# Performance work log

Measured on AMD Instinct MI355X. Metric: run time of the kernel, lower is better.

Reference implementation:

```python
import jax, jax.numpy as jnp
import numpy as np

B, L, D, R = 8, 2048, 2048, 256
K = R if R % 2 == 1 else (R - 1 if R > 1 else 1)  # torch kernel-size rule -> 255


def setup_inputs() -> dict:
    key = jax.random.key(0)
    ks = jax.random.split(key, 6)
    x = jax.random.normal(ks[0], (B, L, D), dtype=jnp.float32)
    ln_gamma = jnp.ones((D,), jnp.float32)
    ln_beta = jnp.zeros((D,), jnp.float32)
    P_shared = jax.random.normal(ks[1], (D, R), jnp.float32) / np.float32(np.sqrt(D))
    dlt_T = jax.random.normal(ks[2], (R, R), jnp.float32) / np.float32(np.sqrt(R))
    phi_w = jax.random.normal(ks[3], (R,), jnp.float32)  # nn.Linear(1, r, bias=False) weight
    phi_bias = jnp.zeros((L, R), jnp.float32)            # created as zeros_like(phi_det)
    toep_params = jnp.ones((K,), jnp.float32) / np.float32(K)
    Wq = jax.random.normal(ks[4], (R, D), jnp.float32) / np.float32(np.sqrt(R))  # delta_Q: r->d
    bq = jnp.zeros((D,), jnp.float32)
    g_logit = jnp.array([-1.0, 0.0], jnp.float32)
    return {"x": x, "ln_gamma": ln_gamma, "ln_beta": ln_beta, "P_shared": P_shared,
            "dlt_T": dlt_T, "phi_w": phi_w, "phi_bias": phi_bias,
            "toep_params": toep_params, "Wq": Wq, "bq": bq, "g_logit": g_logit,
            "step": 5000}


def _layernorm(x, g, b, eps=1e-5):
    m = jnp.mean(x, -1, keepdims=True)
    v = jnp.mean((x - m) ** 2, -1, keepdims=True)
    return (x - m) * jax.lax.rsqrt(v + eps) * g + b


def _phi_det(Ll, Rr, dtype):
    # assumed phi_logic(t, L, r): DCT-II style deterministic phase table, shape (L, r)
    t = jnp.arange(Ll, dtype=dtype)[:, None]
    k = jnp.arange(Rr, dtype=dtype)[None, :]
    return jnp.cos(jnp.pi * (t + 0.5) * k / Ll)


def reference(x, ln_gamma, ln_beta, P_shared, dlt_T, phi_w, phi_bias,
              toep_params, Wq, bq, g_logit, step):
    Bb, Ll, Dd = x.shape
    Rr = P_shared.shape[1]
    x_norm = _layernorm(x, ln_gamma, ln_beta)
    phi_det = _phi_det(Ll, Rr, x.dtype)                      # (L, r)
    feat = jnp.mean(x_norm, -1, keepdims=True)               # (B, L, 1)
    phi_data = jnp.mean(feat * phi_w[None, None, :], axis=0)  # (L, r)
    det_scale = min(step / 2000.0, 1.0)                      # static Python scalar
    phi = det_scale * phi_det + phi_bias + phi_data          # (L, r)
    scale = jnp.sum(phi, axis=1) / jnp.float32(Rr)           # (L,)
    u = jnp.einsum('bld,dr->blr', x_norm, P_shared)          # SharedProj.forward_P
    z = jnp.einsum('blr,sr->bls', u, dlt_T)                  # DLT: fixed spectral transform
    # Toeplitz conv1d across spectral channels, padding 'same' (cross-correlation, as torch)
    zf = z.reshape(Bb * Ll, 1, Rr)
    mixed = jax.lax.conv_general_dilated(zf, toep_params[None, None, :], (1,), 'SAME',
                                         dimension_numbers=('NCH', 'OIH', 'NCH'))
    z_mixed = mixed.reshape(Bb, Ll, Rr)
    y = jnp.einsum('blr,rd->bld', z_mixed, Wq) + bq          # delta_Q
    g = jax.nn.sigmoid(g_logit)
    g = jnp.repeat(g, Dd // g.shape[0])                      # repeat_interleave to d_model
    # scale has L elements, broadcast over the FEATURE dim (L == d_model by construction)
    return g[None, None, :] * y * scale[None, None, :]
```

## Files before the change

kernel.cpp:

```cpp
#include <hip/hip_runtime.h>
#include <cstdint>
#include <math.h>

#define B_ 8
#define L_ 2048
#define D_ 2048
#define R_ 256

typedef __bf16 bf16x8 __attribute__((ext_vector_type(8)));
typedef float f32x4 __attribute__((ext_vector_type(4)));

__device__ __forceinline__ unsigned short f2bf(float f) {
    uint32_t u = __builtin_bit_cast(uint32_t, f);
    u += 0x7FFFu + ((u >> 16) & 1u);
    return (unsigned short)(u >> 16);
}

#define GLDS16(gp, lp)                                                          \
    __builtin_amdgcn_global_load_lds(                                           \
        (const __attribute__((address_space(1))) void*)(gp),                    \
        (__attribute__((address_space(3))) void*)(lp), 16, 0, 0)

__global__ __launch_bounds__(256) void ln_kernel(
    const float* __restrict__ x, const float* __restrict__ gamma,
    const float* __restrict__ beta, unsigned short* __restrict__ xn,
    float* __restrict__ feat)
{
    const int row  = blockIdx.x;
    const int t    = threadIdx.x;
    const int w    = t >> 6, lane = t & 63;
    const float4* x4 = (const float4*)(x + (size_t)row * D_);
    float4 a = x4[t];
    float4 b = x4[t + 256];
    float s  = a.x + a.y + a.z + a.w + b.x + b.y + b.z + b.w;
    float sq = a.x*a.x + a.y*a.y + a.z*a.z + a.w*a.w
             + b.x*b.x + b.y*b.y + b.z*b.z + b.w*b.w;
    __shared__ float red[12];
#pragma unroll
    for (int o = 32; o; o >>= 1) { s += __shfl_down(s, o); sq += __shfl_down(sq, o); }
    if (lane == 0) { red[w] = s; red[4 + w] = sq; }
    __syncthreads();
    float S    = red[0] + red[1] + red[2] + red[3];
    float SQ   = red[4] + red[5] + red[6] + red[7];
    float mean = S * (1.0f / D_);
    float var  = SQ * (1.0f / D_) - mean * mean;
    float rstd = rsqrtf(var + 1e-5f);

    const float4* g4 = (const float4*)gamma;
    const float4* b4 = (const float4*)beta;
    float4 g0 = g4[t], g1 = g4[t + 256];
    float4 e0 = b4[t], e1 = b4[t + 256];

    float n[8];
    n[0] = (a.x - mean) * rstd * g0.x + e0.x;
    n[1] = (a.y - mean) * rstd * g0.y + e0.y;
    n[2] = (a.z - mean) * rstd * g0.z + e0.z;
    n[3] = (a.w - mean) * rstd * g0.w + e0.w;
    n[4] = (b.x - mean) * rstd * g1.x + e1.x;
    n[5] = (b.y - mean) * rstd * g1.y + e1.y;
    n[6] = (b.z - mean) * rstd * g1.z + e1.z;
    n[7] = (b.w - mean) * rstd * g1.w + e1.w;

    ushort4 o0, o1;
    o0.x = f2bf(n[0]); o0.y = f2bf(n[1]); o0.z = f2bf(n[2]); o0.w = f2bf(n[3]);
    o1.x = f2bf(n[4]); o1.y = f2bf(n[5]); o1.z = f2bf(n[6]); o1.w = f2bf(n[7]);
    ((ushort4*)(xn + (size_t)row * D_))[t]       = o0;
    ((ushort4*)(xn + (size_t)row * D_))[t + 256] = o1;

    float fs = n[0]+n[1]+n[2]+n[3]+n[4]+n[5]+n[6]+n[7];
#pragma unroll
    for (int o = 32; o; o >>= 1) fs += __shfl_down(fs, o);
    if (lane == 0) red[8 + w] = fs;
    __syncthreads();
    if (t == 0) feat[row] = (red[8] + red[9] + red[10] + red[11]) * (1.0f / D_);
}

__global__ __launch_bounds__(256) void pt_kernel(
    const float* __restrict__ P, unsigned short* __restrict__ PT)
{
    int k = blockIdx.x;
    int r = threadIdx.x;
    PT[(size_t)r * D_ + k] = f2bf(P[(size_t)k * R_ + r]);
}

__global__ __launch_bounds__(256) void w2_kernel(
    const float* __restrict__ dlt, const float* __restrict__ toep,
    float* __restrict__ W2T)
{
    int s = blockIdx.x, q = threadIdx.x;
    int r0 = s - 127; if (r0 < 0) r0 = 0;
    int r1 = s + 127; if (r1 > 255) r1 = 255;
    float acc = 0.f;
    for (int r = r0; r <= r1; r++)
        acc += dlt[(size_t)r * R_ + q] * toep[r - s + 127];
    W2T[(size_t)s * R_ + q] = acc;
}

__global__ __launch_bounds__(256) void wt_kernel(
    const float* __restrict__ W2T, const float* __restrict__ Wq,
    unsigned short* __restrict__ WT)
{
    int d = blockIdx.x, q = threadIdx.x;
    float acc = 0.f;
    for (int s = 0; s < R_; s++)
        acc += W2T[(size_t)s * R_ + q] * Wq[(size_t)s * D_ + d];
    WT[(size_t)d * R_ + q] = f2bf(acc);
}

__global__ __launch_bounds__(256) void scale_kernel(
    const float* __restrict__ phi_bias, const float* __restrict__ phi_w,
    const float* __restrict__ feat, const float* __restrict__ bq,
    const float* __restrict__ g_logit, const int* __restrict__ step,
    float* __restrict__ gs, float* __restrict__ bgs)
{
    int l = blockIdx.x, k = threadIdx.x;
    int w = k >> 6, lane = k & 63;
    double arg = 3.14159265358979323846 * ((double)l + 0.5) * (double)k / (double)L_;
    float cv = (float)cos(arg);
    float pb = phi_bias[(size_t)l * R_ + k];
    float pw = phi_w[k];
    __shared__ float red[12];
#pragma unroll
    for (int o = 32; o; o >>= 1) {
        cv += __shfl_down(cv, o);
        pb += __shfl_down(pb, o);
        pw += __shfl_down(pw, o);
    }
    if (lane == 0) { red[w] = cv; red[4 + w] = pb; red[8 + w] = pw; }
    __syncthreads();
    if (k == 0) {
        float cs  = red[0] + red[1] + red[2] + red[3];
        float pbs = red[4] + red[5] + red[6] + red[7];
        float pws = red[8] + red[9] + red[10] + red[11];
        float fb = 0.f;
        for (int b = 0; b < B_; b++) fb += feat[(size_t)b * L_ + l];
        fb *= (1.0f / B_);
        float det = fminf((float)step[0] / 2000.0f, 1.0f);
        float sc  = (det * cs + pbs + fb * pws) * (1.0f / R_);
        float gl  = g_logit[l >> 10];
        float gg  = 1.0f / (1.0f + expf(-gl));
        gs[l]  = gg * sc;
        bgs[l] = bq[l] * gg * sc;
    }
}

__global__ __launch_bounds__(256, 2) void gemm1_kernel(
    const unsigned short* __restrict__ A,
    const unsigned short* __restrict__ BT,
    unsigned short* __restrict__ U)
{
    __shared__ __align__(16) unsigned short sA[64 * 32];
    __shared__ __align__(16) unsigned short sB[128 * 32];
    const int tid  = threadIdx.x;
    const int m0   = blockIdx.x * 64;
    const int n0   = blockIdx.y * 128;
    const int w    = tid >> 6, lane = tid & 63;
    const int quad = lane >> 4, m16 = lane & 15;
    const int wm   = (w >> 1) * 32, wn = (w & 1) * 64;

    f32x4 acc[2][4] = {};

    for (int kc = 0; kc < 2048; kc += 32) {
        {
            int r = tid >> 2, seg = tid & 3;
            GLDS16(A + (size_t)(m0 + r) * 2048 + kc + seg * 8, sA + tid * 8);
        }
#pragma unroll
        for (int i = 0; i < 2; i++) {
            int idx = i * 256 + tid;
            int r = idx >> 2, seg = idx & 3;
            GLDS16(BT + (size_t)(n0 + r) * 2048 + kc + seg * 8, sB + idx * 8);
        }
        __syncthreads();
        bf16x8 af[2], bf[4];
#pragma unroll
        for (int i = 0; i < 2; i++)
            af[i] = *(const bf16x8*)(sA + ((wm + i * 16 + m16) * 32 + quad * 8));
#pragma unroll
        for (int j = 0; j < 4; j++)
            bf[j] = *(const bf16x8*)(sB + ((wn + j * 16 + m16) * 32 + quad * 8));
#pragma unroll
        for (int i = 0; i < 2; i++)
#pragma unroll
            for (int j = 0; j < 4; j++)
                acc[i][j] = __builtin_amdgcn_mfma_f32_16x16x32_bf16(
                    af[i], bf[j], acc[i][j], 0, 0, 0);
        __syncthreads();
    }

#pragma unroll
    for (int i = 0; i < 2; i++)
#pragma unroll
        for (int j = 0; j < 4; j++) {
            int col = n0 + wn + j * 16 + m16;
#pragma unroll
            for (int r = 0; r < 4; r++) {
                int row = m0 + wm + i * 16 + quad * 4 + r;
                U[(size_t)row * 256 + col] = f2bf(acc[i][j][r]);
            }
        }
}

__global__ __launch_bounds__(256, 2) void gemm2_kernel(
    const unsigned short* __restrict__ A,
    const unsigned short* __restrict__ BT,
    const float* __restrict__ gs, const float* __restrict__ bgs,
    float* __restrict__ out)
{
    __shared__ __align__(16) unsigned short sA[128 * 32];
    __shared__ __align__(16) unsigned short sB[128 * 32];
    const int tid  = threadIdx.x;
    const int m0   = blockIdx.x * 128;
    const int n0   = blockIdx.y * 128;
    const int w    = tid >> 6, lane = tid & 63;
    const int quad = lane >> 4, m16 = lane & 15;
    const int wm   = (w >> 1) * 64, wn = (w & 1) * 64;

    f32x4 acc[4][4] = {};

    for (int kc = 0; kc < 256; kc += 32) {
#pragma unroll
        for (int i = 0; i < 2; i++) {
            int idx = i * 256 + tid;
            int r = idx >> 2, seg = idx & 3;
            GLDS16(A + (size_t)(m0 + r) * 256 + kc + seg * 8, sA + idx * 8);
            GLDS16(BT + (size_t)(n0 + r) * 256 + kc + seg * 8, sB + idx * 8);
        }
        __syncthreads();
        bf16x8 af[4], bf[4];
#pragma unroll
        for (int i = 0; i < 4; i++)
            af[i] = *(const bf16x8*)(sA + ((wm + i * 16 + m16) * 32 + quad * 8));
#pragma unroll
        for (int j = 0; j < 4; j++)
            bf[j] = *(const bf16x8*)(sB + ((wn + j * 16 + m16) * 32 + quad * 8));
#pragma unroll
        for (int i = 0; i < 4; i++)
#pragma unroll
            for (int j = 0; j < 4; j++)
                acc[i][j] = __builtin_amdgcn_mfma_f32_16x16x32_bf16(
                    af[i], bf[j], acc[i][j], 0, 0, 0);
        __syncthreads();
    }

#pragma unroll
    for (int j = 0; j < 4; j++) {
        int col = n0 + wn + j * 16 + m16;
        float gv = gs[col], bv = bgs[col];
#pragma unroll
        for (int i = 0; i < 4; i++)
#pragma unroll
            for (int r = 0; r < 4; r++) {
                int row = m0 + wm + i * 16 + quad * 4 + r;
                out[(size_t)row * 2048 + col] = acc[i][j][r] * gv + bv;
            }
    }
}

extern "C" void kernel_launch(void* const* d_in, const int* in_sizes, int n_in,
                              void* d_out, int out_size, void* d_ws, size_t ws_size,
                              hipStream_t stream)
{
    const float* x        = (const float*)d_in[0];
    const float* ln_gamma = (const float*)d_in[1];
    const float* ln_beta  = (const float*)d_in[2];
    const float* P        = (const float*)d_in[3];
    const float* dlt      = (const float*)d_in[4];
    const float* phi_w    = (const float*)d_in[5];
    const float* phi_bias = (const float*)d_in[6];
    const float* toep     = (const float*)d_in[7];
    const float* Wq       = (const float*)d_in[8];
    const float* bq       = (const float*)d_in[9];
    const float* g_logit  = (const float*)d_in[10];
    const int*   step     = (const int*)d_in[11];
    float* out = (float*)d_out;

    char* w = (char*)d_ws;
    unsigned short* xn  = (unsigned short*)(w);
    unsigned short* u   = (unsigned short*)(w + 67108864);
    unsigned short* PT  = (unsigned short*)(w + 75497472);
    unsigned short* WT  = (unsigned short*)(w + 76546048);
    float*          W2T = (float*)(w + 77594624);
    float*          feat= (float*)(w + 77856768);
    float*          gs  = (float*)(w + 77922304);
    float*          bgs = (float*)(w + 77930496);

    ln_kernel<<<dim3(B_ * L_), dim3(256), 0, stream>>>(x, ln_gamma, ln_beta, xn, feat);
    pt_kernel<<<dim3(D_), dim3(256), 0, stream>>>(P, PT);
    w2_kernel<<<dim3(R_), dim3(256), 0, stream>>>(dlt, toep, W2T);
    wt_kernel<<<dim3(D_), dim3(256), 0, stream>>>(W2T, Wq, WT);
    scale_kernel<<<dim3(L_), dim3(256), 0, stream>>>(phi_bias, phi_w, feat, bq,
                                                     g_logit, step, gs, bgs);
    gemm1_kernel<<<dim3(256, 2), dim3(256), 0, stream>>>(xn, PT, u);
    gemm2_kernel<<<dim3(128, 16), dim3(256), 0, stream>>>(u, WT, gs, bgs, out);
}
```

Before: 421.3 us.

## Rework LayerNorm reduction, transpose, weight prep and GEMM K-stepping

LayerNorm now computes the normalized-row mean algebraically from extra reductions in the first pass, which removes the second reduction and barrier. The P transpose goes through shared memory with vectorized stores, and the weight-fold kernel computes four outputs per thread. The scale kernel uses float cos instead of double. Both GEMMs now load two K slices of 32 per barrier and swap the grid axes so neighbouring blocks share A rows. gemm2 raises its occupancy hint and hoists the epilogue scale loads ahead of the main loop.

```diff
diff --git a/kernel.cpp b/kernel.cpp
--- a/kernel.cpp
+++ b/kernel.cpp
@@ -30,26 +30,44 @@
     const int t    = threadIdx.x;
     const int w    = t >> 6, lane = t & 63;
     const float4* x4 = (const float4*)(x + (size_t)row * D_);
-    float4 a = x4[t];
-    float4 b = x4[t + 256];
-    float s  = a.x + a.y + a.z + a.w + b.x + b.y + b.z + b.w;
-    float sq = a.x*a.x + a.y*a.y + a.z*a.z + a.w*a.w
-             + b.x*b.x + b.y*b.y + b.z*b.z + b.w*b.w;
-    __shared__ float red[12];
-#pragma unroll
-    for (int o = 32; o; o >>= 1) { s += __shfl_down(s, o); sq += __shfl_down(sq, o); }
-    if (lane == 0) { red[w] = s; red[4 + w] = sq; }
+    const float4* g4 = (const float4*)gamma;
+    const float4* b4 = (const float4*)beta;
+    float4 a  = x4[t];
+    float4 b  = x4[t + 256];
+    float4 g0 = g4[t], g1 = g4[t + 256];
+    float4 e0 = b4[t], e1 = b4[t + 256];
+
+    float s   = a.x + a.y + a.z + a.w + b.x + b.y + b.z + b.w;
+    float sq  = a.x*a.x + a.y*a.y + a.z*a.z + a.w*a.w
+              + b.x*b.x + b.y*b.y + b.z*b.z + b.w*b.w;
+    float sxg = a.x*g0.x + a.y*g0.y + a.z*g0.z + a.w*g0.w
+              + b.x*g1.x + b.y*g1.y + b.z*g1.z + b.w*g1.w;
+    float sg  = g0.x + g0.y + g0.z + g0.w + g1.x + g1.y + g1.z + g1.w;
+    float sb  = e0.x + e0.y + e0.z + e0.w + e1.x + e1.y + e1.z + e1.w;
+
+    __shared__ float red[20];
+#pragma unroll
+    for (int o = 32; o; o >>= 1) {
+        s   += __shfl_down(s, o);
+        sq  += __shfl_down(sq, o);
+        sxg += __shfl_down(sxg, o);
+        sg  += __shfl_down(sg, o);
+        sb  += __shfl_down(sb, o);
+    }
+    if (lane == 0) {
+        red[w] = s; red[4+w] = sq; red[8+w] = sxg; red[12+w] = sg; red[16+w] = sb;
+    }
     __syncthreads();
     float S    = red[0] + red[1] + red[2] + red[3];
     float SQ   = red[4] + red[5] + red[6] + red[7];
+    float SXG  = red[8] + red[9] + red[10] + red[11];
+    float SG   = red[12] + red[13] + red[14] + red[15];
+    float SB   = red[16] + red[17] + red[18] + red[19];
     float mean = S * (1.0f / D_);
     float var  = SQ * (1.0f / D_) - mean * mean;
     float rstd = rsqrtf(var + 1e-5f);
-
-    const float4* g4 = (const float4*)gamma;
-    const float4* b4 = (const float4*)beta;
-    float4 g0 = g4[t], g1 = g4[t + 256];
-    float4 e0 = b4[t], e1 = b4[t + 256];
+    if (t == 0)
+        feat[row] = (rstd * (SXG - mean * SG) + SB) * (1.0f / D_);
 
     float n[8];
     n[0] = (a.x - mean) * rstd * g0.x + e0.x;
@@ -66,21 +84,26 @@
     o1.x = f2bf(n[4]); o1.y = f2bf(n[5]); o1.z = f2bf(n[6]); o1.w = f2bf(n[7]);
     ((ushort4*)(xn + (size_t)row * D_))[t]       = o0;
     ((ushort4*)(xn + (size_t)row * D_))[t + 256] = o1;
-
-    float fs = n[0]+n[1]+n[2]+n[3]+n[4]+n[5]+n[6]+n[7];
-#pragma unroll
-    for (int o = 32; o; o >>= 1) fs += __shfl_down(fs, o);
-    if (lane == 0) red[8 + w] = fs;
-    __syncthreads();
-    if (t == 0) feat[row] = (red[8] + red[9] + red[10] + red[11]) * (1.0f / D_);
 }
 
 __global__ __launch_bounds__(256) void pt_kernel(
     const float* __restrict__ P, unsigned short* __restrict__ PT)
 {
-    int k = blockIdx.x;
-    int r = threadIdx.x;
-    PT[(size_t)r * D_ + k] = f2bf(P[(size_t)k * R_ + r]);
+    __shared__ unsigned short sT[64 * 256];
+    const int k0 = blockIdx.x * 64, t = threadIdx.x;
+#pragma unroll 8
+    for (int j = 0; j < 64; j++)
+        sT[j * 256 + t] = f2bf(P[(size_t)(k0 + j) * R_ + t]);
+    __syncthreads();
+#pragma unroll
+    for (int c = 0; c < 16; c++) {
+        ushort4 v;
+        v.x = sT[(c * 4 + 0) * 256 + t];
+        v.y = sT[(c * 4 + 1) * 256 + t];
+        v.z = sT[(c * 4 + 2) * 256 + t];
+        v.w = sT[(c * 4 + 3) * 256 + t];
+        *(ushort4*)(PT + (size_t)t * D_ + k0 + c * 4) = v;
+    }
 }
 
 __global__ __launch_bounds__(256) void w2_kernel(
@@ -100,11 +123,17 @@
     const float* __restrict__ W2T, const float* __restrict__ Wq,
     unsigned short* __restrict__ WT)
 {
-    int d = blockIdx.x, q = threadIdx.x;
-    float acc = 0.f;
-    for (int s = 0; s < R_; s++)
-        acc += W2T[(size_t)s * R_ + q] * Wq[(size_t)s * D_ + d];
-    WT[(size_t)d * R_ + q] = f2bf(acc);
+    const int d0 = blockIdx.x * 4, q = threadIdx.x;
+    float a0 = 0.f, a1 = 0.f, a2 = 0.f, a3 = 0.f;
+    for (int s = 0; s < R_; s++) {
+        float w2 = W2T[(size_t)s * R_ + q];
+        const float* wr = Wq + (size_t)s * D_ + d0;
+        a0 += w2 * wr[0]; a1 += w2 * wr[1]; a2 += w2 * wr[2]; a3 += w2 * wr[3];
+    }
+    WT[(size_t)(d0 + 0) * R_ + q] = f2bf(a0);
+    WT[(size_t)(d0 + 1) * R_ + q] = f2bf(a1);
+    WT[(size_t)(d0 + 2) * R_ + q] = f2bf(a2);
+    WT[(size_t)(d0 + 3) * R_ + q] = f2bf(a3);
 }
 
 __global__ __launch_bounds__(256) void scale_kernel(
@@ -115,8 +144,8 @@
 {
     int l = blockIdx.x, k = threadIdx.x;
     int w = k >> 6, lane = k & 63;
-    double arg = 3.14159265358979323846 * ((double)l + 0.5) * (double)k / (double)L_;
-    float cv = (float)cos(arg);
+    float arg = 3.14159265358979323846f * ((float)l + 0.5f) * (float)k * (1.0f / L_);
+    float cv = cosf(arg);
     float pb = phi_bias[(size_t)l * R_ + k];
     float pw = phi_w[k];
     __shared__ float red[12];
@@ -149,42 +178,47 @@
     const unsigned short* __restrict__ BT,
     unsigned short* __restrict__ U)
 {
-    __shared__ __align__(16) unsigned short sA[64 * 32];
-    __shared__ __align__(16) unsigned short sB[128 * 32];
+    __shared__ __align__(16) unsigned short sA[2][64 * 32];
+    __shared__ __align__(16) unsigned short sB[2][128 * 32];
     const int tid  = threadIdx.x;
-    const int m0   = blockIdx.x * 64;
-    const int n0   = blockIdx.y * 128;
+    const int n0   = blockIdx.x * 128;
+    const int m0   = blockIdx.y * 64;
     const int w    = tid >> 6, lane = tid & 63;
     const int quad = lane >> 4, m16 = lane & 15;
     const int wm   = (w >> 1) * 32, wn = (w & 1) * 64;
+    const int ra   = tid >> 2, sa = tid & 3;
 
     f32x4 acc[2][4] = {};
 
-    for (int kc = 0; kc < 2048; kc += 32) {
-        {
-            int r = tid >> 2, seg = tid & 3;
-            GLDS16(A + (size_t)(m0 + r) * 2048 + kc + seg * 8, sA + tid * 8);
-        }
+    for (int kc = 0; kc < 2048; kc += 64) {
+        const unsigned short* ap = A + (size_t)(m0 + ra) * 2048 + kc + sa * 8;
+        GLDS16(ap,      sA[0] + tid * 8);
+        GLDS16(ap + 32, sA[1] + tid * 8);
 #pragma unroll
         for (int i = 0; i < 2; i++) {
             int idx = i * 256 + tid;
             int r = idx >> 2, seg = idx & 3;
-            GLDS16(BT + (size_t)(n0 + r) * 2048 + kc + seg * 8, sB + idx * 8);
+            const unsigned short* bp = BT + (size_t)(n0 + r) * 2048 + kc + seg * 8;
+            GLDS16(bp,      sB[0] + idx * 8);
+            GLDS16(bp + 32, sB[1] + idx * 8);
         }
         __syncthreads();
-        bf16x8 af[2], bf[4];
-#pragma unroll
-        for (int i = 0; i < 2; i++)
-            af[i] = *(const bf16x8*)(sA + ((wm + i * 16 + m16) * 32 + quad * 8));
-#pragma unroll
-        for (int j = 0; j < 4; j++)
-            bf[j] = *(const bf16x8*)(sB + ((wn + j * 16 + m16) * 32 + quad * 8));
-#pragma unroll
-        for (int i = 0; i < 2; i++)
+#pragma unroll
+        for (int h = 0; h < 2; h++) {
+            bf16x8 af[2], bf[4];
+#pragma unroll
+            for (int i = 0; i < 2; i++)
+                af[i] = *(const bf16x8*)(sA[h] + ((wm + i * 16 + m16) * 32 + quad * 8));
 #pragma unroll
             for (int j = 0; j < 4; j++)
-                acc[i][j] = __builtin_amdgcn_mfma_f32_16x16x32_bf16(
-                    af[i], bf[j], acc[i][j], 0, 0, 0);
+                bf[j] = *(const bf16x8*)(sB[h] + ((wn + j * 16 + m16) * 32 + quad * 8));
+#pragma unroll
+            for (int i = 0; i < 2; i++)
+#pragma unroll
+                for (int j = 0; j < 4; j++)
+                    acc[i][j] = __builtin_amdgcn_mfma_f32_16x16x32_bf16(
+                        af[i], bf[j], acc[i][j], 0, 0, 0);
+        }
         __syncthreads();
     }
 
@@ -201,60 +235,73 @@
         }
 }
 
-__global__ __launch_bounds__(256, 2) void gemm2_kernel(
+__global__ __launch_bounds__(256, 3) void gemm2_kernel(
     const unsigned short* __restrict__ A,
     const unsigned short* __restrict__ BT,
     const float* __restrict__ gs, const float* __restrict__ bgs,
     float* __restrict__ out)
 {
-    __shared__ __align__(16) unsigned short sA[128 * 32];
-    __shared__ __align__(16) unsigned short sB[128 * 32];
+    __shared__ __align__(16) unsigned short sA[2][128 * 32];
+    __shared__ __align__(16) unsigned short sB[2][128 * 32];
     const int tid  = threadIdx.x;
-    const int m0   = blockIdx.x * 128;
-    const int n0   = blockIdx.y * 128;
+    const int n0   = blockIdx.x * 128;
+    const int m0   = blockIdx.y * 128;
     const int w    = tid >> 6, lane = tid & 63;
     const int quad = lane >> 4, m16 = lane & 15;
     const int wm   = (w >> 1) * 64, wn = (w & 1) * 64;
 
+    float gv[4], bv[4];
+#pragma unroll
+    for (int j = 0; j < 4; j++) {
+        int col = n0 + wn + j * 16 + m16;
+        gv[j] = gs[col];
+        bv[j] = bgs[col];
+    }
+
     f32x4 acc[4][4] = {};
 
-    for (int kc = 0; kc < 256; kc += 32) {
+    for (int kc = 0; kc < 256; kc += 64) {
 #pragma unroll
         for (int i = 0; i < 2; i++) {
             int idx = i * 256 + tid;
             int r = idx >> 2, seg = idx & 3;
-            GLDS16(A + (size_t)(m0 + r) * 256 + kc + seg * 8, sA + idx * 8);
-            GLDS16(BT + (size_t)(n0 + r) * 256 + kc + seg * 8, sB + idx * 8);
+            const unsigned short* ap = A + (size_t)(m0 + r) * 256 + kc + seg * 8;
+            const unsigned short* bp = BT + (size_t)(n0 + r) * 256 + kc + seg * 8;
+            GLDS16(ap,      sA[0] + idx * 8);
+            GLDS16(ap + 32, sA[1] + idx * 8);
+            GLDS16(bp,      sB[0] + idx * 8);
+            GLDS16(bp + 32, sB[1] + idx * 8);
         }
         __syncthreads();
-        bf16x8 af[4], bf[4];
-#pragma unroll
-        for (int i = 0; i < 4; i++)
-            af[i] = *(const bf16x8*)(sA + ((wm + i * 16 + m16) * 32 + quad * 8));
-#pragma unroll
-        for (int j = 0; j < 4; j++)
-            bf[j] = *(const bf16x8*)(sB + ((wn + j * 16 + m16) * 32 + quad * 8));
-#pragma unroll
-        for (int i = 0; i < 4; i++)
+#pragma unroll
+        for (int h = 0; h < 2; h++) {
+            bf16x8 af[4], bf[4];
+#pragma unroll
+            for (int i = 0; i < 4; i++)
+                af[i] = *(const bf16x8*)(sA[h] + ((wm + i * 16 + m16) * 32 + quad * 8));
 #pragma unroll
             for (int j = 0; j < 4; j++)
-                acc[i][j] = __builtin_amdgcn_mfma_f32_16x16x32_bf16(
-                    af[i], bf[j], acc[i][j], 0, 0, 0);
+                bf[j] = *(const bf16x8*)(sB[h] + ((wn + j * 16 + m16) * 32 + quad * 8));
+#pragma unroll
+            for (int i = 0; i < 4; i++)
+#pragma unroll
+                for (int j = 0; j < 4; j++)
+                    acc[i][j] = __builtin_amdgcn_mfma_f32_16x16x32_bf16(
+                        af[i], bf[j], acc[i][j], 0, 0, 0);
+        }
         __syncthreads();
     }
 
 #pragma unroll
-    for (int j = 0; j < 4; j++) {
-        int col = n0 + wn + j * 16 + m16;
-        float gv = gs[col], bv = bgs[col];
-#pragma unroll
-        for (int i = 0; i < 4; i++)
-#pragma unroll
-            for (int r = 0; r < 4; r++) {
-                int row = m0 + wm + i * 16 + quad * 4 + r;
-                out[(size_t)row * 2048 + col] = acc[i][j][r] * gv + bv;
-            }
-    }
+    for (int i = 0; i < 4; i++)
+#pragma unroll
+        for (int r = 0; r < 4; r++) {
+            int row = m0 + wm + i * 16 + quad * 4 + r;
+            float* op = out + (size_t)row * 2048 + n0 + wn;
+#pragma unroll
+            for (int j = 0; j < 4; j++)
+                op[j * 16 + m16] = acc[i][j][r] * gv[j] + bv[j];
+        }
 }
 
 extern "C" void kernel_launch(void* const* d_in, const int* in_sizes, int n_in,
@@ -286,11 +333,11 @@
     float*          bgs = (float*)(w + 77930496);
 
     ln_kernel<<<dim3(B_ * L_), dim3(256), 0, stream>>>(x, ln_gamma, ln_beta, xn, feat);
-    pt_kernel<<<dim3(D_), dim3(256), 0, stream>>>(P, PT);
+    pt_kernel<<<dim3(32), dim3(256), 0, stream>>>(P, PT);
     w2_kernel<<<dim3(R_), dim3(256), 0, stream>>>(dlt, toep, W2T);
-    wt_kernel<<<dim3(D_), dim3(256), 0, stream>>>(W2T, Wq, WT);
+    wt_kernel<<<dim3(512), dim3(256), 0, stream>>>(W2T, Wq, WT);
     scale_kernel<<<dim3(L_), dim3(256), 0, stream>>>(phi_bias, phi_w, feat, bq,
                                                      g_logit, step, gs, bgs);
-    gemm1_kernel<<<dim3(256, 2), dim3(256), 0, stream>>>(xn, PT, u);
-    gemm2_kernel<<<dim3(128, 16), dim3(256), 0, stream>>>(u, WT, gs, bgs, out);
-}
+    gemm1_kernel<<<dim3(2, 256), dim3(256), 0, stream>>>(xn, PT, u);
+    gemm2_kernel<<<dim3(16, 128), dim3(256), 0, stream>>>(u, WT, gs, bgs, out);
+}
```

After: 397.2 us. 1.06x faster.
